# Optimization experiments

Measured on AMD Instinct MI355X. Metric: run time of the kernel, lower is better.

## Reference

```python
import jax, jax.numpy as jnp
import numpy as np

N_ATOMS = 50000
IN_DIM = 128
HID = 256
N_ELEM = 4
N_IMG = 500
NNZ = 2_000_000
ELEMENTS = jnp.array([1, 6, 8, 29], dtype=jnp.int64)


def setup_inputs() -> dict:
    key = jax.random.key(0)
    ks = jax.random.split(key, 14)
    fingerprints = jax.random.normal(ks[0], (N_ATOMS, IN_DIM), dtype=jnp.float32)
    # atomic numbers drawn from the supported element set
    elem_idx = jax.random.randint(ks[1], (N_ATOMS,), 0, N_ELEM)
    atomic_numbers = ELEMENTS[elem_idx]
    image_idx = jnp.sort(jax.random.randint(ks[2], (N_ATOMS,), 0, N_IMG))
    # sparse fprimes (COO): [N_ATOMS*IN_DIM, 3*N_ATOMS]
    fprime_rows = jax.random.randint(ks[3], (NNZ,), 0, N_ATOMS * IN_DIM)
    fprime_cols = jax.random.randint(ks[4], (NNZ,), 0, 3 * N_ATOMS)
    fprime_vals = jax.random.normal(ks[5], (NNZ,), dtype=jnp.float32) * 0.1
    # per-element MLP params, stacked over the element axis (torch Linear-style init)
    s0, s1 = 1.0 / np.sqrt(IN_DIM), 1.0 / np.sqrt(HID)
    W0 = jax.random.uniform(ks[6], (N_ELEM, IN_DIM, HID), jnp.float32, -s0, s0)
    b0 = jax.random.uniform(ks[7], (N_ELEM, HID), jnp.float32, -s0, s0)
    W1 = jax.random.uniform(ks[8], (N_ELEM, HID, HID), jnp.float32, -s1, s1)
    b1 = jax.random.uniform(ks[9], (N_ELEM, HID), jnp.float32, -s1, s1)
    W2 = jax.random.uniform(ks[10], (N_ELEM, HID, 1), jnp.float32, -s1, s1)
    b2 = jax.random.uniform(ks[11], (N_ELEM, 1), jnp.float32, -s1, s1)
    return {"fingerprints": fingerprints, "atomic_numbers": atomic_numbers,
            "image_idx": image_idx, "fprime_rows": fprime_rows,
            "fprime_cols": fprime_cols, "fprime_vals": fprime_vals,
            "W0": W0, "b0": b0, "W1": W1, "b1": b1, "W2": W2, "b2": b2}


def _per_atom_energy(fp, atomic_numbers, W0, b0, W1, b1, W2, b2):
    # Run every element-specific MLP over ALL atoms (as the torch module does),
    # then mask by the one-hot element membership and sum over elements.
    h = jnp.tanh(jnp.einsum('nd,edh->enh', fp, W0) + b0[:, None, :])   # [E,N,H]
    h = jnp.tanh(jnp.einsum('enh,ehk->enk', h, W1) + b1[:, None, :])   # [E,N,H]
    out = jnp.einsum('enh,eho->eno', h, W2) + b2[:, None, :]           # [E,N,1]
    mask = (atomic_numbers[None, :] == ELEMENTS[:, None]).astype(fp.dtype)  # [E,N]
    return jnp.sum(mask * out[..., 0], axis=0)                          # [N]


def reference(fingerprints, atomic_numbers, image_idx, fprime_rows,
              fprime_cols, fprime_vals, W0, b0, W1, b1, W2, b2):
    o = _per_atom_energy(fingerprints, atomic_numbers, W0, b0, W1, b1, W2, b2)
    energy = jax.ops.segment_sum(o, image_idx, num_segments=N_IMG)  # [N_IMG]
    # dE/dfp for forces (sum over images == sum over atoms of o)
    g = jax.grad(lambda fp: jnp.sum(
        _per_atom_energy(fp, atomic_numbers, W0, b0, W1, b1, W2, b2)))(fingerprints)
    g_flat = g.reshape(-1)  # [N*D]
    # forces = -fprimes^T @ g_flat, fprimes in COO form
    forces = -jax.ops.segment_sum(fprime_vals * g_flat[fprime_rows],
                                  fprime_cols, num_segments=3 * N_ATOMS)
    return energy, forces.reshape(N_ATOMS, 3)
```

## Files before the change

kernel.cpp:

```cpp
#include <hip/hip_runtime.h>
#include <math.h>

#define N_ATOMS 50000
#define IN_DIM 128
#define HID 256
#define N_ELEM 4
#define N_IMG 500
#define NNZ 2000000

#define CBINS 293
#define CW 512
#define BCAP 8192
#define OCAP 4096
#define CSPLIT 2
#define PCH 2560
#define NBP ((NNZ + PCH - 1) / PCH)
#define NFB 2048
#define TOTB (NBP + NFB)
#define BKB ((N_ATOMS + 255) / 256)
#define PREPB 384

typedef __attribute__((ext_vector_type(8))) short bf16x8;
typedef __attribute__((ext_vector_type(4))) float f32x4;
typedef __attribute__((ext_vector_type(4))) int   i32x4;
typedef __attribute__((ext_vector_type(4))) float fv4;

__device__ __forceinline__ int elem_of(int z) {
    return (z == 1) ? 0 : (z == 6) ? 1 : (z == 8) ? 2 : 3;
}

__device__ __forceinline__ unsigned short f2bf(float f) {
    unsigned u = __float_as_uint(f);
    u += 0x7fffu + ((u >> 16) & 1u);
    return (unsigned short)(u >> 16);
}
__device__ __forceinline__ float bf2f(unsigned short u) {
    return __uint_as_float(((unsigned)u) << 16);
}
__device__ __forceinline__ float tanh_fast(float x) {
    float e = __expf(2.f * x);
    return (e - 1.f) / (e + 1.f);
}

__global__ __launch_bounds__(256) void prep_and_bucket(
    const float* __restrict__ W0, const float* __restrict__ W1,
    unsigned short* __restrict__ W0s1,
    unsigned short* __restrict__ W1s2,
    unsigned short* __restrict__ W1s3,
    unsigned short* __restrict__ W0s4,
    const int* __restrict__ Z, int* __restrict__ counts,
    int* __restrict__ lists, float* __restrict__ F) {

    const int tid = threadIdx.x;

    if (blockIdx.x >= PREPB) {
        __shared__ int lcnt[N_ELEM], lbase[N_ELEM];
        const int bb = blockIdx.x - PREPB;
        for (int idx = bb * 256 + tid; idx < 3 * N_ATOMS; idx += BKB * 256)
            F[idx] = 0.f;
        const int i = bb * 256 + tid;
        if (tid < N_ELEM) lcnt[tid] = 0;
        __syncthreads();
        int e = -1, pos = 0;
        if (i < N_ATOMS) {
            e = elem_of(Z[i]);
            pos = atomicAdd(&lcnt[e], 1);
        }
        __syncthreads();
        if (tid < N_ELEM) lbase[tid] = atomicAdd(&counts[tid], lcnt[tid]);
        __syncthreads();
        if (i < N_ATOMS) lists[e * N_ATOMS + lbase[e] + pos] = i;
        return;
    }

    const int T = blockIdx.x * 256 + tid;

    if (T < 32768) {
        const int e = T >> 13, fid = T & 8191;
        const int blkv = fid >> 6, lane = fid & 63;
        const int k0 = ((blkv & 7) << 5) | ((lane >> 4) << 3);
        const int n  = ((blkv >> 3) << 4) | (lane & 15);
        const float* src = W1 + e * 65536 + n;
        bf16x8 vv;
#pragma unroll
        for (int j = 0; j < 8; ++j) vv[j] = (short)f2bf(src[(k0 + j) * 256]);
        *(bf16x8*)(W1s2 + (e << 16) + (fid << 3)) = vv;
    } else if (T < 65536) {
        const int u = T - 32768, e = u >> 13, fid = u & 8191;
        const int blkv = fid >> 6, lane = fid & 63;
        const int k  = ((blkv >> 3) << 4) | (lane & 15);
        const int n0 = ((blkv & 7) << 5) | ((lane >> 4) << 3);
        const float* src = W1 + e * 65536 + k * 256 + n0;
        float4 a = *(const float4*)src;
        float4 b = *(const float4*)(src + 4);
        bf16x8 vv;
        vv[0] = (short)f2bf(a.x); vv[1] = (short)f2bf(a.y);
        vv[2] = (short)f2bf(a.z); vv[3] = (short)f2bf(a.w);
        vv[4] = (short)f2bf(b.x); vv[5] = (short)f2bf(b.y);
        vv[6] = (short)f2bf(b.z); vv[7] = (short)f2bf(b.w);
        *(bf16x8*)(W1s3 + (e << 16) + (fid << 3)) = vv;
    } else if (T < 81920) {
        const int u = T - 65536, e = u >> 12, fid = u & 4095;
        const int blkv = fid >> 6, lane = fid & 63;
        const int k0 = ((blkv & 3) << 5) | ((lane >> 4) << 3);
        const int n  = ((blkv >> 2) << 4) | (lane & 15);
        const float* src = W0 + e * 32768 + n;
        bf16x8 vv;
#pragma unroll
        for (int j = 0; j < 8; ++j) vv[j] = (short)f2bf(src[(k0 + j) * 256]);
        *(bf16x8*)(W0s1 + e * 32768 + (fid << 3)) = vv;
    } else if (T < 98304) {
        const int u = T - 81920, e = u >> 12, fid = u & 4095;
        const int blkv = fid >> 6, lane = fid & 63;
        const int k  = ((blkv >> 3) << 4) | (lane & 15);
        const int n0 = ((blkv & 7) << 5) | ((lane >> 4) << 3);
        const float* src = W0 + e * 32768 + k * 256 + n0;
        float4 a = *(const float4*)src;
        float4 b = *(const float4*)(src + 4);
        bf16x8 vv;
        vv[0] = (short)f2bf(a.x); vv[1] = (short)f2bf(a.y);
        vv[2] = (short)f2bf(a.z); vv[3] = (short)f2bf(a.w);
        vv[4] = (short)f2bf(b.x); vv[5] = (short)f2bf(b.y);
        vv[6] = (short)f2bf(b.z); vv[7] = (short)f2bf(b.w);
        *(bf16x8*)(W0s4 + e * 32768 + (fid << 3)) = vv;
    }
}

#define TILES_PER_E 512
#define CH 1280
__global__ __launch_bounds__(256, 4) void mega_mlp_bin(
    const float* __restrict__ fp,
    const unsigned short* __restrict__ W0s1,
    const unsigned short* __restrict__ W1s2,
    const unsigned short* __restrict__ W1s3,
    const unsigned short* __restrict__ W0s4,
    const float* __restrict__ b0, const float* __restrict__ b1,
    const float* __restrict__ W2, const float* __restrict__ b2,
    float* __restrict__ o_atom,
    unsigned short* __restrict__ Gb,
    const int* __restrict__ counts, const int* __restrict__ lists,
    const int* __restrict__ rows, const int* __restrict__ cols,
    const float* __restrict__ vals,
    unsigned* __restrict__ packB, float* __restrict__ valsB,
    int* __restrict__ gcur,
    int* __restrict__ ovfR, int* __restrict__ ovfC, float* __restrict__ ovfV,
    int* __restrict__ ocur) {

    __shared__ __align__(16) char smem[40960];
    const int tid = threadIdx.x;

    const int bid = blockIdx.x;
    const int pA = (bid * NBP) / TOTB;
    const int pB = ((bid + 1) * NBP) / TOTB;

    if (pB > pA) {
        int*   Lr    = (int*)smem;
        int*   Lc    = (int*)(smem + 10240);
        float* Lv    = (float*)(smem + 20480);
        int*   hist  = (int*)(smem + 30720);
        int*   pref  = (int*)(smem + 31892);
        int*   curs  = (int*)(smem + 33064);
        int*   gbase = (int*)(smem + 34236);

        const int base = pA * PCH;
        const int lim = (base + PCH <= NNZ) ? PCH : (NNZ - base);

        for (int i = tid; i < CBINS; i += 256) hist[i] = 0;
        __syncthreads();

        i32x4 r[3], c[3];
        fv4   v[3];
        int nvalid[3];
#pragma unroll
        for (int j = 0; j < 3; ++j) {
            const int li = tid * 4 + 1024 * j;
            const int i0 = base + li;
            int nv = lim - li;
            nvalid[j] = nv > 4 ? 4 : (nv < 0 ? 0 : nv);
            if (nvalid[j] == 4) {
                r[j] = __builtin_nontemporal_load((const i32x4*)(rows + i0));
                c[j] = __builtin_nontemporal_load((const i32x4*)(cols + i0));
                v[j] = __builtin_nontemporal_load((const fv4*)(vals + i0));
            } else {
                for (int e2 = 0; e2 < nvalid[j]; ++e2) {
                    r[j][e2] = rows[i0 + e2]; c[j][e2] = cols[i0 + e2];
                    v[j][e2] = vals[i0 + e2];
                }
            }
#pragma unroll
            for (int e2 = 0; e2 < 4; ++e2)
                if (e2 < nvalid[j]) atomicAdd(&hist[c[j][e2] >> 9], 1);
        }
        __syncthreads();

        if (tid == 0) {
            int s = 0;
            for (int b = 0; b < CBINS; ++b) { pref[b] = s; s += hist[b]; }
        }
        __syncthreads();
        for (int b = tid; b < CBINS; b += 256) {
            gbase[b] = atomicAdd(&gcur[b], hist[b]);
            curs[b] = pref[b];
        }
        __syncthreads();

#pragma unroll
        for (int j = 0; j < 3; ++j)
#pragma unroll
            for (int e2 = 0; e2 < 4; ++e2)
                if (e2 < nvalid[j]) {
                    int b = c[j][e2] >> 9;
                    int p = atomicAdd(&curs[b], 1);
                    Lr[p] = r[j][e2]; Lc[p] = c[j][e2]; Lv[p] = v[j][e2];
                }
        __syncthreads();

#pragma unroll
        for (int j = 0; j < 10; ++j) {
            const int p = tid + 256 * j;
            if (p >= lim) break;
            const int col = Lc[p];
            const int b = col >> 9;
            const int g = gbase[b] + (p - pref[b]);
            if (g < BCAP) {
                packB[b * BCAP + g] = ((unsigned)(col & 511) << 23) | (unsigned)Lr[p];
                valsB[b * BCAP + g] = Lv[p];
            } else {
                int od = atomicAdd(ocur, 1);
                if (od < OCAP) { ovfR[od] = Lr[p]; ovfC[od] = col; ovfV[od] = Lv[p]; }
            }
        }
        return;
    }

    const int fid = bid - pB;
    const int xcd = fid & 7;
    const int e = xcd & 3;
    const int tile = (fid >> 3) * 2 + (xcd >> 2);
    const int cnt = counts[e];
    const int m0 = tile * 32;
    if (m0 >= cnt) return;
    const int* list = lists + e * N_ATOMS;

    short* tH = (short*)smem;
    short* tD = (short*)(smem + 20480);

    const int lane = tid & 63;
    const int wv = tid >> 6;
    const int lr = lane & 15;
    const int lq = lane >> 4;

    const unsigned short* B1 = W0s1 + (size_t)e * HID * IN_DIM;
    const unsigned short* B2 = W1s2 + (size_t)e * HID * HID;
    const unsigned short* B3 = W1s3 + (size_t)e * HID * HID;
    const unsigned short* B4 = W0s4 + (size_t)e * IN_DIM * HID;

    f32x4 acc[2][4];
#define ZERO_ACC()                                                        \
    _Pragma("unroll") for (int mt = 0; mt < 2; ++mt)                      \
        _Pragma("unroll") for (int nt = 0; nt < 4; ++nt)                  \
            _Pragma("unroll") for (int j = 0; j < 4; ++j) acc[mt][nt][j] = 0.f;

    {
        bf16x8 bb0[4];
#pragma unroll
        for (int nt = 0; nt < 4; ++nt)
            bb0[nt] = *(const bf16x8*)(B1 +
                ((size_t)(((wv * 4 + nt) * 4 + 0) * 64 + lane) << 3));

#pragma unroll
        for (int p = 0; p < 4; ++p) {
            const int row = p * 8 + (tid >> 5);
            const int col = (tid & 31) * 4;
            const int m = m0 + row;
            float4 a = make_float4(0.f, 0.f, 0.f, 0.f);
            if (m < cnt)
                a = *(const float4*)(fp + (size_t)list[m] * IN_DIM + col);
            short4 b;
            b.x = (short)f2bf(a.x); b.y = (short)f2bf(a.y);
            b.z = (short)f2bf(a.z); b.w = (short)f2bf(a.w);
            *(short4*)&tD[(col >> 5) * CH + row * 40 + (col & 31)] = b;
        }
        __syncthreads();

        ZERO_ACC();
        bf16x8 bb[2][4];
#pragma unroll
        for (int nt = 0; nt < 4; ++nt) bb[0][nt] = bb0[nt];
#pragma unroll
        for (int ki = 0; ki < 4; ++ki) {
            const int cur = ki & 1, nx = cur ^ 1;
            if (ki < 3) {
#pragma unroll
                for (int nt = 0; nt < 4; ++nt)
                    bb[nx][nt] = *(const bf16x8*)(B1 +
                        ((size_t)(((wv * 4 + nt) * 4 + ki + 1) * 64 + lane) << 3));
            }
            bf16x8 af[2];
#pragma unroll
            for (int mt = 0; mt < 2; ++mt)
                af[mt] = *(const bf16x8*)&tD[ki * CH + (mt * 16 + lr) * 40 + lq * 8];
#pragma unroll
            for (int mt = 0; mt < 2; ++mt)
#pragma unroll
                for (int nt = 0; nt < 4; ++nt)
                    acc[mt][nt] = __builtin_amdgcn_mfma_f32_16x16x32_bf16(
                        af[mt], bb[cur][nt], acc[mt][nt], 0, 0, 0);
        }
    }

    bf16x8 b2r[3][4];
#pragma unroll
    for (int p = 0; p < 3; ++p)
#pragma unroll
        for (int nt = 0; nt < 4; ++nt)
            b2r[p][nt] = *(const bf16x8*)(B2 +
                ((size_t)(((wv * 4 + nt) * 8 + p) * 64 + lane) << 3));

    {
        float bv[4];
#pragma unroll
        for (int nt = 0; nt < 4; ++nt)
            bv[nt] = b0[e * HID + wv * 64 + nt * 16 + lr];
#pragma unroll
        for (int mt = 0; mt < 2; ++mt)
#pragma unroll
            for (int rr = 0; rr < 4; ++rr) {
                const int row = mt * 16 + lq * 4 + rr;
#pragma unroll
                for (int nt = 0; nt < 4; ++nt) {
                    const int n = wv * 64 + nt * 16 + lr;
                    float t = tanh_fast(acc[mt][nt][rr] + bv[nt]);
                    tH[(n >> 5) * CH + row * 40 + (n & 31)] = (short)f2bf(t);
                }
            }
    }
    __syncthreads();

    ZERO_ACC();
#pragma unroll
    for (int ki = 0; ki < 8; ++ki) {
        bf16x8 af[2];
#pragma unroll
        for (int mt = 0; mt < 2; ++mt)
            af[mt] = *(const bf16x8*)&tH[ki * CH + (mt * 16 + lr) * 40 + lq * 8];
#pragma unroll
        for (int mt = 0; mt < 2; ++mt)
#pragma unroll
            for (int nt = 0; nt < 4; ++nt)
                acc[mt][nt] = __builtin_amdgcn_mfma_f32_16x16x32_bf16(
                    af[mt], b2r[ki % 3][nt], acc[mt][nt], 0, 0, 0);
        if (ki < 5) {
#pragma unroll
            for (int nt = 0; nt < 4; ++nt)
                b2r[ki % 3][nt] = *(const bf16x8*)(B2 +
                    ((size_t)(((wv * 4 + nt) * 8 + ki + 3) * 64 + lane) << 3));
        }
    }

    bf16x8 b3r[3][4];
#pragma unroll
    for (int p = 0; p < 3; ++p)
#pragma unroll
        for (int nt = 0; nt < 4; ++nt)
            b3r[p][nt] = *(const bf16x8*)(B3 +
                ((size_t)(((wv * 4 + nt) * 8 + p) * 64 + lane) << 3));

    {
        float bv[4], w2v[4];
#pragma unroll
        for (int nt = 0; nt < 4; ++nt) {
            bv[nt]  = b1[e * HID + wv * 64 + nt * 16 + lr];
            w2v[nt] = W2[e * HID + wv * 64 + nt * 16 + lr];
        }
#pragma unroll
        for (int mt = 0; mt < 2; ++mt)
#pragma unroll
            for (int rr = 0; rr < 4; ++rr) {
                const int row = mt * 16 + lq * 4 + rr;
                float osum = 0.f;
#pragma unroll
                for (int nt = 0; nt < 4; ++nt) {
                    const int n = wv * 64 + nt * 16 + lr;
                    float t = tanh_fast(acc[mt][nt][rr] + bv[nt]);
                    osum += t * w2v[nt];
                    tD[(n >> 5) * CH + row * 40 + (n & 31)] =
                        (short)f2bf(w2v[nt] * (1.f - t * t));
                }
                osum += __shfl_xor(osum, 1, 64);
                osum += __shfl_xor(osum, 2, 64);
                osum += __shfl_xor(osum, 4, 64);
                osum += __shfl_xor(osum, 8, 64);
                if (lr == 0)
                    ((float*)&tD[row * 40 + 32])[wv] = osum;
            }
    }
    __syncthreads();
    if (tid < 32) {
        int m = m0 + tid;
        if (m < cnt) {
            const float4 r4 = *(const float4*)&tD[tid * 40 + 32];
            o_atom[list[m]] = r4.x + r4.y + r4.z + r4.w + b2[e];
        }
    }

    ZERO_ACC();
#pragma unroll
    for (int ki = 0; ki < 8; ++ki) {
        bf16x8 af[2];
#pragma unroll
        for (int mt = 0; mt < 2; ++mt)
            af[mt] = *(const bf16x8*)&tD[ki * CH + (mt * 16 + lr) * 40 + lq * 8];
#pragma unroll
        for (int mt = 0; mt < 2; ++mt)
#pragma unroll
            for (int nt = 0; nt < 4; ++nt)
                acc[mt][nt] = __builtin_amdgcn_mfma_f32_16x16x32_bf16(
                    af[mt], b3r[ki % 3][nt], acc[mt][nt], 0, 0, 0);
        if (ki < 5) {
#pragma unroll
            for (int nt = 0; nt < 4; ++nt)
                b3r[ki % 3][nt] = *(const bf16x8*)(B3 +
                    ((size_t)(((wv * 4 + nt) * 8 + ki + 3) * 64 + lane) << 3));
        }
    }

    bf16x8 b4r[3][2];
#pragma unroll
    for (int p = 0; p < 3; ++p)
#pragma unroll
        for (int nt = 0; nt < 2; ++nt)
            b4r[p][nt] = *(const bf16x8*)(B4 +
                ((size_t)(((wv * 2 + nt) * 8 + p) * 64 + lane) << 3));

#pragma unroll
    for (int mt = 0; mt < 2; ++mt)
#pragma unroll
        for (int rr = 0; rr < 4; ++rr) {
            const int row = mt * 16 + lq * 4 + rr;
#pragma unroll
            for (int nt = 0; nt < 4; ++nt) {
                const int n = wv * 64 + nt * 16 + lr;
                const int a = (n >> 5) * CH + row * 40 + (n & 31);
                float h = bf2f((unsigned short)tH[a]);
                tH[a] = (short)f2bf(acc[mt][nt][rr] * (1.f - h * h));
            }
        }
    __syncthreads();

    {
        f32x4 a4[2][2];
#pragma unroll
        for (int mt = 0; mt < 2; ++mt)
#pragma unroll
            for (int nt = 0; nt < 2; ++nt)
#pragma unroll
                for (int j = 0; j < 4; ++j) a4[mt][nt][j] = 0.f;
#pragma unroll
        for (int ki = 0; ki < 8; ++ki) {
            bf16x8 af[2];
#pragma unroll
            for (int mt = 0; mt < 2; ++mt)
                af[mt] = *(const bf16x8*)&tH[ki * CH + (mt * 16 + lr) * 40 + lq * 8];
#pragma unroll
            for (int mt = 0; mt < 2; ++mt)
#pragma unroll
                for (int nt = 0; nt < 2; ++nt)
                    a4[mt][nt] = __builtin_amdgcn_mfma_f32_16x16x32_bf16(
                        af[mt], b4r[ki % 3][nt], a4[mt][nt], 0, 0, 0);
            if (ki < 5) {
#pragma unroll
                for (int nt = 0; nt < 2; ++nt)
                    b4r[ki % 3][nt] = *(const bf16x8*)(B4 +
                        ((size_t)(((wv * 2 + nt) * 8 + ki + 3) * 64 + lane) << 3));
            }
        }
#pragma unroll
        for (int mt = 0; mt < 2; ++mt)
#pragma unroll
            for (int rr = 0; rr < 4; ++rr) {
                const int row = mt * 16 + lq * 4 + rr;
#pragma unroll
                for (int nt = 0; nt < 2; ++nt) {
                    const int n = wv * 32 + nt * 16 + lr;
                    tD[(n >> 5) * CH + row * 40 + (n & 31)] =
                        (short)f2bf(a4[mt][nt][rr]);
                }
            }
    }
    __syncthreads();
#pragma unroll
    for (int t = 0; t < 2; ++t) {
        const int c = tid + 256 * t;
        const int row = c >> 4;
        const int pos = (c & 15) * 8;
        const int m = m0 + row;
        if (m < cnt) {
            bf16x8 v = *(const bf16x8*)&tD[(pos >> 5) * CH + row * 40 + (pos & 31)];
            *(bf16x8*)(Gb + (size_t)list[m] * IN_DIM + pos) = v;
        }
    }
#undef ZERO_ACC
}

__global__ __launch_bounds__(1024) void forces_consumer(
    const unsigned* __restrict__ packB, const float* __restrict__ valsB,
    const int* __restrict__ gcur,
    const unsigned short* __restrict__ g, float* __restrict__ F,
    const float* __restrict__ o_atom, const int* __restrict__ img,
    float* __restrict__ energy,
    const int* __restrict__ ovfR, const int* __restrict__ ovfC,
    const float* __restrict__ ovfV, const int* __restrict__ ocur) {

    const int blk = blockIdx.x;

    if (blk < CBINS * CSPLIT) {
        __shared__ float win[CW];
        const int w = blk / CSPLIT, half = blk % CSPLIT;
        for (int i = threadIdx.x; i < CW; i += 1024) win[i] = 0.f;
        __syncthreads();
        const int w0 = w << 9;
        int cnt = gcur[w]; if (cnt > BCAP) cnt = BCAP;
        const size_t o = (size_t)w * BCAP;
        for (int idx0 = (int)threadIdx.x * 4 + half * 4096; idx0 < cnt;
             idx0 += 4096 * CSPLIT) {
            if (idx0 + 4 <= cnt) {
                i32x4 p = *(const i32x4*)((const int*)packB + o + idx0);
                fv4   v = *(const fv4*)(valsB + o + idx0);
                unsigned p0 = (unsigned)p[0], p1 = (unsigned)p[1];
                unsigned p2 = (unsigned)p[2], p3 = (unsigned)p[3];
                float g0 = bf2f(g[p0 & 0x7FFFFFu]), g1 = bf2f(g[p1 & 0x7FFFFFu]);
                float g2 = bf2f(g[p2 & 0x7FFFFFu]), g3 = bf2f(g[p3 & 0x7FFFFFu]);
                atomicAdd(&win[p0 >> 23], -v[0] * g0);
                atomicAdd(&win[p1 >> 23], -v[1] * g1);
                atomicAdd(&win[p2 >> 23], -v[2] * g2);
                atomicAdd(&win[p3 >> 23], -v[3] * g3);
            } else {
                for (int e2 = idx0; e2 < cnt; ++e2) {
                    unsigned p0 = packB[o + e2];
                    atomicAdd(&win[p0 >> 23],
                              -valsB[o + e2] * bf2f(g[p0 & 0x7FFFFFu]));
                }
            }
        }
        if (half == 0) {
            int ocnt = ocur[0]; if (ocnt > OCAP) ocnt = OCAP;
            for (int k2 = threadIdx.x; k2 < ocnt; k2 += 1024) {
                int c = ovfC[k2];
                if (c >= w0 && c < w0 + CW)
                    atomicAdd(&win[c - w0], -ovfV[k2] * bf2f(g[ovfR[k2]]));
            }
        }
        __syncthreads();
        for (int i = threadIdx.x; i < CW; i += 1024) {
            int c = w0 + i;
            if (c < 3 * N_ATOMS) atomicAdd(&F[c], win[i]);
        }
        return;
    }

    {
        const int bb = blk - CBINS * CSPLIT;
        int lo, hi;
        {
            int l = 0, r = N_ATOMS;
            while (l < r) { int m = (l + r) >> 1; if (img[m] < bb) l = m + 1; else r = m; }
            lo = l;
        }
        {
            int l = lo, r = N_ATOMS;
            while (l < r) { int m = (l + r) >> 1; if (img[m] < bb + 1) l = m + 1; else r = m; }
            hi = l;
        }
        float s = 0.f;
        for (int i2 = lo + (int)threadIdx.x; i2 < hi; i2 += 1024) s += o_atom[i2];
#pragma unroll
        for (int off = 32; off > 0; off >>= 1) s += __shfl_down(s, off, 64);
        __shared__ float red[16];
        if ((threadIdx.x & 63) == 0) red[threadIdx.x >> 6] = s;
        __syncthreads();
        if (threadIdx.x == 0) {
            float t = 0.f;
#pragma unroll
            for (int w2 = 0; w2 < 16; ++w2) t += red[w2];
            energy[bb] = t;
        }
    }
}

extern "C" void kernel_launch(void* const* d_in, const int* in_sizes, int n_in,
                              void* d_out, int out_size, void* d_ws, size_t ws_size,
                              hipStream_t stream) {
    const float* fp    = (const float*)d_in[0];
    const int*   Z     = (const int*)d_in[1];
    const int*   img   = (const int*)d_in[2];
    const int*   frows = (const int*)d_in[3];
    const int*   fcols = (const int*)d_in[4];
    const float* fvals = (const float*)d_in[5];
    const float* W0    = (const float*)d_in[6];
    const float* b0    = (const float*)d_in[7];
    const float* W1    = (const float*)d_in[8];
    const float* b1    = (const float*)d_in[9];
    const float* W2    = (const float*)d_in[10];
    const float* b2    = (const float*)d_in[11];

    float* out    = (float*)d_out;
    float* energy = out;
    float* F      = out + N_IMG;

    char* ws = (char*)d_ws;
    int*   counts = (int*)ws;
    int*   gcur   = (int*)(ws + 32);
    int*   ocur   = (int*)(ws + 32 + 4 * CBINS);
    int*   lists  = (int*)(ws + 4096);
    char*  base   = ws + (1 << 20);
    unsigned short* Gb   = (unsigned short*)(base);
    float* o_atom        = (float*)(base + 13000000);
    unsigned short* W0s1 = (unsigned short*)(base + 14000000);
    unsigned short* W0s4 = W0s1 + N_ELEM * IN_DIM * HID;
    unsigned short* W1s2 = W0s4 + N_ELEM * IN_DIM * HID;
    unsigned short* W1s3 = W1s2 + N_ELEM * HID * HID;
    unsigned* packB = (unsigned*)(base + 19000000);
    float* valsB = (float*)(base + 29000000);
    int*   ovfR  = (int*)(base + 49000000);
    int*   ovfC  = (int*)(base + 49050000);
    float* ovfV  = (float*)(base + 49100000);

    hipMemsetAsync(ws, 0, 32 + 4 * CBINS + 4, stream);

    prep_and_bucket<<<PREPB + BKB, 256, 0, stream>>>(
        W0, W1, W0s1, W1s2, W1s3, W0s4, Z, counts, lists, F);

    mega_mlp_bin<<<TOTB, 256, 0, stream>>>(
        fp, W0s1, W1s2, W1s3, W0s4, b0, b1, W2, b2, o_atom, Gb, counts, lists,
        frows, fcols, fvals, packB, valsB, gcur, ovfR, ovfC, ovfV, ocur);

    forces_consumer<<<CBINS * CSPLIT + N_IMG, 1024, 0, stream>>>(
        packB, valsB, gcur, Gb, F, o_atom, img, energy,
        ovfR, ovfC, ovfV, ocur);
}
```

Measured before the change: 196.0 us.

## Bucket sparse fprime entries by row and scatter directly to global forces

Sparse entries are now binned by fingerprint row (16384-row bins) instead of force column. Each consumer block then reads a localized slice of the gradient buffer, which should improve cache locality for the g gather. Results go straight to global F through atomics instead of a shared-memory window, and the consumer uses 256-thread blocks split four ways per bin. Overflow entries get their own block. The cost is far more global atomic traffic to scattered force addresses, and the smaller bin capacity (6144 per bin) could spill into the overflow path more often.

```diff
diff --git a/kernel.cpp b/kernel.cpp
--- a/kernel.cpp
+++ b/kernel.cpp
@@ -8,11 +8,11 @@
 #define N_IMG 500
 #define NNZ 2000000
 
-#define CBINS 293
-#define CW 512
-#define BCAP 8192
+#define RBINS 391
+#define BCAP 6144
 #define OCAP 4096
-#define CSPLIT 2
+#define SPLIT 4
+#define CONS_B (RBINS * SPLIT)
 #define PCH 2560
 #define NBP ((NNZ + PCH - 1) / PCH)
 #define NFB 2048
@@ -158,14 +158,14 @@
         int*   Lc    = (int*)(smem + 10240);
         float* Lv    = (float*)(smem + 20480);
         int*   hist  = (int*)(smem + 30720);
-        int*   pref  = (int*)(smem + 31892);
-        int*   curs  = (int*)(smem + 33064);
-        int*   gbase = (int*)(smem + 34236);
+        int*   pref  = (int*)(smem + 32284);
+        int*   curs  = (int*)(smem + 33848);
+        int*   gbase = (int*)(smem + 35412);
 
         const int base = pA * PCH;
         const int lim = (base + PCH <= NNZ) ? PCH : (NNZ - base);
 
-        for (int i = tid; i < CBINS; i += 256) hist[i] = 0;
+        for (int i = tid; i < RBINS; i += 256) hist[i] = 0;
         __syncthreads();
 
         i32x4 r[3], c[3];
@@ -189,16 +189,16 @@
             }
 #pragma unroll
             for (int e2 = 0; e2 < 4; ++e2)
-                if (e2 < nvalid[j]) atomicAdd(&hist[c[j][e2] >> 9], 1);
+                if (e2 < nvalid[j]) atomicAdd(&hist[r[j][e2] >> 14], 1);
         }
         __syncthreads();
 
         if (tid == 0) {
             int s = 0;
-            for (int b = 0; b < CBINS; ++b) { pref[b] = s; s += hist[b]; }
-        }
-        __syncthreads();
-        for (int b = tid; b < CBINS; b += 256) {
+            for (int b = 0; b < RBINS; ++b) { pref[b] = s; s += hist[b]; }
+        }
+        __syncthreads();
+        for (int b = tid; b < RBINS; b += 256) {
             gbase[b] = atomicAdd(&gcur[b], hist[b]);
             curs[b] = pref[b];
         }
@@ -209,7 +209,7 @@
 #pragma unroll
             for (int e2 = 0; e2 < 4; ++e2)
                 if (e2 < nvalid[j]) {
-                    int b = c[j][e2] >> 9;
+                    int b = r[j][e2] >> 14;
                     int p = atomicAdd(&curs[b], 1);
                     Lr[p] = r[j][e2]; Lc[p] = c[j][e2]; Lv[p] = v[j][e2];
                 }
@@ -219,15 +219,16 @@
         for (int j = 0; j < 10; ++j) {
             const int p = tid + 256 * j;
             if (p >= lim) break;
-            const int col = Lc[p];
-            const int b = col >> 9;
+            const int row = Lr[p];
+            const int b = row >> 14;
             const int g = gbase[b] + (p - pref[b]);
             if (g < BCAP) {
-                packB[b * BCAP + g] = ((unsigned)(col & 511) << 23) | (unsigned)Lr[p];
+                packB[b * BCAP + g] =
+                    ((unsigned)(row & 16383) << 18) | (unsigned)Lc[p];
                 valsB[b * BCAP + g] = Lv[p];
             } else {
                 int od = atomicAdd(ocur, 1);
-                if (od < OCAP) { ovfR[od] = Lr[p]; ovfC[od] = col; ovfV[od] = Lv[p]; }
+                if (od < OCAP) { ovfR[od] = row; ovfC[od] = Lc[p]; ovfV[od] = Lv[p]; }
             }
         }
         return;
@@ -503,7 +504,7 @@
 #undef ZERO_ACC
 }
 
-__global__ __launch_bounds__(1024) void forces_consumer(
+__global__ __launch_bounds__(256) void forces_consumer(
     const unsigned* __restrict__ packB, const float* __restrict__ valsB,
     const int* __restrict__ gcur,
     const unsigned short* __restrict__ g, float* __restrict__ F,
@@ -513,54 +514,39 @@
     const float* __restrict__ ovfV, const int* __restrict__ ocur) {
 
     const int blk = blockIdx.x;
-
-    if (blk < CBINS * CSPLIT) {
-        __shared__ float win[CW];
-        const int w = blk / CSPLIT, half = blk % CSPLIT;
-        for (int i = threadIdx.x; i < CW; i += 1024) win[i] = 0.f;
-        __syncthreads();
-        const int w0 = w << 9;
-        int cnt = gcur[w]; if (cnt > BCAP) cnt = BCAP;
-        const size_t o = (size_t)w * BCAP;
-        for (int idx0 = (int)threadIdx.x * 4 + half * 4096; idx0 < cnt;
-             idx0 += 4096 * CSPLIT) {
-            if (idx0 + 4 <= cnt) {
-                i32x4 p = *(const i32x4*)((const int*)packB + o + idx0);
-                fv4   v = *(const fv4*)(valsB + o + idx0);
-                unsigned p0 = (unsigned)p[0], p1 = (unsigned)p[1];
-                unsigned p2 = (unsigned)p[2], p3 = (unsigned)p[3];
-                float g0 = bf2f(g[p0 & 0x7FFFFFu]), g1 = bf2f(g[p1 & 0x7FFFFFu]);
-                float g2 = bf2f(g[p2 & 0x7FFFFFu]), g3 = bf2f(g[p3 & 0x7FFFFFu]);
-                atomicAdd(&win[p0 >> 23], -v[0] * g0);
-                atomicAdd(&win[p1 >> 23], -v[1] * g1);
-                atomicAdd(&win[p2 >> 23], -v[2] * g2);
-                atomicAdd(&win[p3 >> 23], -v[3] * g3);
+    const int tid = threadIdx.x;
+
+    if (blk < CONS_B) {
+        const int bin = blk >> 2, sl = blk & 3;
+        int cnt = gcur[bin]; if (cnt > BCAP) cnt = BCAP;
+        int per = ((cnt + SPLIT - 1) / SPLIT + 3) & ~3;
+        const int lo = sl * per;
+        int hi = lo + per; if (hi > cnt) hi = cnt;
+        const size_t o = (size_t)bin * BCAP;
+        const int rbase = bin << 14;
+        for (int i0 = lo + tid * 4; i0 < hi; i0 += 1024) {
+            if (i0 + 4 <= hi) {
+                i32x4 p = *(const i32x4*)((const int*)packB + o + i0);
+                fv4   v = *(const fv4*)(valsB + o + i0);
+#pragma unroll
+                for (int e2 = 0; e2 < 4; ++e2) {
+                    unsigned pk = (unsigned)p[e2];
+                    float gv = bf2f(g[rbase | (int)(pk >> 18)]);
+                    atomicAdd(&F[pk & 0x3FFFFu], -v[e2] * gv);
+                }
             } else {
-                for (int e2 = idx0; e2 < cnt; ++e2) {
-                    unsigned p0 = packB[o + e2];
-                    atomicAdd(&win[p0 >> 23],
-                              -valsB[o + e2] * bf2f(g[p0 & 0x7FFFFFu]));
+                for (int e2 = i0; e2 < hi; ++e2) {
+                    unsigned pk = packB[o + e2];
+                    atomicAdd(&F[pk & 0x3FFFFu],
+                              -valsB[o + e2] * bf2f(g[rbase | (int)(pk >> 18)]));
                 }
             }
         }
-        if (half == 0) {
-            int ocnt = ocur[0]; if (ocnt > OCAP) ocnt = OCAP;
-            for (int k2 = threadIdx.x; k2 < ocnt; k2 += 1024) {
-                int c = ovfC[k2];
-                if (c >= w0 && c < w0 + CW)
-                    atomicAdd(&win[c - w0], -ovfV[k2] * bf2f(g[ovfR[k2]]));
-            }
-        }
-        __syncthreads();
-        for (int i = threadIdx.x; i < CW; i += 1024) {
-            int c = w0 + i;
-            if (c < 3 * N_ATOMS) atomicAdd(&F[c], win[i]);
-        }
         return;
     }
 
-    {
-        const int bb = blk - CBINS * CSPLIT;
+    if (blk < CONS_B + N_IMG) {
+        const int bb = blk - CONS_B;
         int lo, hi;
         {
             int l = 0, r = N_ATOMS;
@@ -573,18 +559,21 @@
             hi = l;
         }
         float s = 0.f;
-        for (int i2 = lo + (int)threadIdx.x; i2 < hi; i2 += 1024) s += o_atom[i2];
+        for (int i2 = lo + tid; i2 < hi; i2 += 256) s += o_atom[i2];
 #pragma unroll
         for (int off = 32; off > 0; off >>= 1) s += __shfl_down(s, off, 64);
-        __shared__ float red[16];
-        if ((threadIdx.x & 63) == 0) red[threadIdx.x >> 6] = s;
-        __syncthreads();
-        if (threadIdx.x == 0) {
-            float t = 0.f;
-#pragma unroll
-            for (int w2 = 0; w2 < 16; ++w2) t += red[w2];
-            energy[bb] = t;
-        }
+        __shared__ float red[4];
+        if ((tid & 63) == 0) red[tid >> 6] = s;
+        __syncthreads();
+        if (tid == 0)
+            energy[bb] = red[0] + red[1] + red[2] + red[3];
+        return;
+    }
+
+    {
+        int ocnt = ocur[0]; if (ocnt > OCAP) ocnt = OCAP;
+        for (int k2 = tid; k2 < ocnt; k2 += 256)
+            atomicAdd(&F[ovfC[k2]], -ovfV[k2] * bf2f(g[ovfR[k2]]));
     }
 }
 
@@ -611,7 +600,7 @@
     char* ws = (char*)d_ws;
     int*   counts = (int*)ws;
     int*   gcur   = (int*)(ws + 32);
-    int*   ocur   = (int*)(ws + 32 + 4 * CBINS);
+    int*   ocur   = (int*)(ws + 32 + 4 * RBINS);
     int*   lists  = (int*)(ws + 4096);
     char*  base   = ws + (1 << 20);
     unsigned short* Gb   = (unsigned short*)(base);
@@ -626,7 +615,7 @@
     int*   ovfC  = (int*)(base + 49050000);
     float* ovfV  = (float*)(base + 49100000);
 
-    hipMemsetAsync(ws, 0, 32 + 4 * CBINS + 4, stream);
+    hipMemsetAsync(ws, 0, 32 + 4 * RBINS + 4, stream);
 
     prep_and_bucket<<<PREPB + BKB, 256, 0, stream>>>(
         W0, W1, W0s1, W1s2, W1s3, W0s4, Z, counts, lists, F);
@@ -635,7 +624,7 @@
         fp, W0s1, W1s2, W1s3, W0s4, b0, b1, W2, b2, o_atom, Gb, counts, lists,
         frows, fcols, fvals, packB, valsB, gcur, ovfR, ovfC, ovfV, ocur);
 
-    forces_consumer<<<CBINS * CSPLIT + N_IMG, 1024, 0, stream>>>(
+    forces_consumer<<<CONS_B + N_IMG + 1, 256, 0, stream>>>(
         packB, valsB, gcur, Gb, F, o_atom, img, energy,
         ovfR, ovfC, ovfV, ocur);
 }
```

Result: slower. 269.9 us (+37.7%).
